# Optimization experiments

Hardware: AMD Instinct MI355X
Metric: run time of the kernel (lower is better)

Reference implementation:

```python
import jax, jax.numpy as jnp
import numpy as np

B, N, D_IN, HID = 8, 2048, 256, 64  # batch, nodes, input hidden, graph hidden (heads=1)
NEG_INF = -9e15  # matches -9000000000000000.0 in the torch code


def setup_inputs() -> dict:
    key = jax.random.key(0)
    k1, k2, k3, k4 = jax.random.split(key, 4)
    node_features = jax.random.normal(k1, (B, N, D_IN), dtype=jnp.float32)
    adj = jax.random.randint(k2, (B, N, N), 0, 2, dtype=jnp.int32)
    W = jax.random.normal(k3, (D_IN, HID), dtype=jnp.float32) / np.sqrt(D_IN).astype(np.float32)
    a = jax.random.normal(k4, (2 * HID, 1), dtype=jnp.float32) * 0.1
    return {"node_features": node_features, "adj": adj, "W": W, "a": a}


def reference(node_features, adj, W, a):
    # Wh = W(node_features): (B, N, HID)
    Wh = jnp.einsum('bnd,dh->bnh', node_features, W)
    a1 = a[:HID, 0]   # attention vector for the 'source' half of the concat
    a2 = a[HID:, 0]   # attention vector for the 'neighbor' half
    f1 = Wh @ a1      # (B, N) = Wh_i . a1
    f2 = Wh @ a2      # (B, N) = Wh_j . a2
    # e_ij = leakyrelu([Wh_i || Wh_j] . a) -- avoids the O(N^2 * 2*HID) concat
    e = jax.nn.leaky_relu(f1[:, :, None] + f2[:, None, :], negative_slope=0.2)  # (B, N, N)
    att = jnp.where(adj > 0, e, jnp.float32(NEG_INF))
    att = jax.nn.softmax(att, axis=2)
    # dropout is identity in eval / with graph_dropout=0.0
    h_prime = jnp.einsum('bij,bjh->bih', att, Wh)  # (B, N, HID)
    return h_prime
```

## Files before the change

### kernel.cpp

```cpp
#include <hip/hip_runtime.h>

#define NB 8
#define NN 2048
#define DIN 256
#define HID 64
#define JSPLIT 8

typedef __bf16 bf16x8_t __attribute__((ext_vector_type(8)));
typedef float f32x16_t __attribute__((ext_vector_type(16)));

__global__ __launch_bounds__(256) void k_wh(
    const float* __restrict__ x, const float* __restrict__ W,
    const float* __restrict__ a,
    __bf16* __restrict__ wht_hi, __bf16* __restrict__ wht_lo,
    float* __restrict__ f1, float* __restrict__ f2)
{
    __shared__ float smem[DIN * 64];
    const int t = threadIdx.x;
    const int g0 = blockIdx.x * 64;
    const int b = g0 >> 11;
    const int n0 = g0 & (NN - 1);

    const float4* x4 = (const float4*)x;
#pragma unroll
    for (int it = 0; it < 16; ++it) {
        int c = t + it * 256;
        int row = c & 63;
        int dg = c >> 6;
        float4 v = x4[(size_t)(g0 + row) * 64 + dg];
        smem[(dg * 4 + 0) * 64 + row] = v.x;
        smem[(dg * 4 + 1) * 64 + row] = v.y;
        smem[(dg * 4 + 2) * 64 + row] = v.z;
        smem[(dg * 4 + 3) * 64 + row] = v.w;
    }
    __syncthreads();

    const int hq = t & 15;
    const int rg = t >> 4;
    const float4* W4 = (const float4*)W;
    float acc[4][4] = {};
#pragma unroll 8
    for (int d = 0; d < DIN; ++d) {
        float4 wv = W4[d * 16 + hq];
        float4 xv = *(const float4*)&smem[d * 64 + rg * 4];
        float xr[4] = {xv.x, xv.y, xv.z, xv.w};
        float wk[4] = {wv.x, wv.y, wv.z, wv.w};
#pragma unroll
        for (int r = 0; r < 4; ++r)
#pragma unroll
            for (int k = 0; k < 4; ++k) acc[r][k] += xr[r] * wk[k];
    }

    float4 a1v = ((const float4*)a)[hq];
    float4 a2v = ((const float4*)a)[16 + hq];
#pragma unroll
    for (int r = 0; r < 4; ++r) {
        float p1 = acc[r][0] * a1v.x + acc[r][1] * a1v.y + acc[r][2] * a1v.z + acc[r][3] * a1v.w;
        float p2 = acc[r][0] * a2v.x + acc[r][1] * a2v.y + acc[r][2] * a2v.z + acc[r][3] * a2v.w;
#pragma unroll
        for (int m = 1; m < 16; m <<= 1) {
            p1 += __shfl_xor(p1, m);
            p2 += __shfl_xor(p2, m);
        }
        if (hq == 0) {
            f1[g0 + rg * 4 + r] = p1;
            f2[g0 + rg * 4 + r] = p2;
        }
    }

    __syncthreads();
#pragma unroll
    for (int r = 0; r < 4; ++r)
#pragma unroll
        for (int k = 0; k < 4; ++k) {
            int h = hq * 4 + k;
            int row = rg * 4 + r;
            smem[h * 64 + (((row >> 2) ^ (h & 15)) << 2) + (row & 3)] = acc[r][k];
        }
    __syncthreads();

    const int h = t >> 2;
    const int rc = t & 3;
    union { __bf16 bh[16]; uint4 u4[2]; } uh, ul;
#pragma unroll
    for (int q = 0; q < 4; ++q) {
        float4 v = *(const float4*)&smem[h * 64 + (((rc * 4 + q) ^ (h & 15)) << 2)];
        float vv[4] = {v.x, v.y, v.z, v.w};
#pragma unroll
        for (int e = 0; e < 4; ++e) {
            float val = vv[e];
            __bf16 hi = (__bf16)val;
            __bf16 lo = (__bf16)(val - (float)hi);
            uh.bh[q * 4 + e] = hi;
            ul.bh[q * 4 + e] = lo;
        }
    }
    size_t obase = (size_t)(b * HID + h) * NN + n0 + rc * 16;
    *(uint4*)&wht_hi[obase] = uh.u4[0];
    *(uint4*)&wht_hi[obase + 8] = uh.u4[1];
    *(uint4*)&wht_lo[obase] = ul.u4[0];
    *(uint4*)&wht_lo[obase + 8] = ul.u4[1];
}

__global__ __launch_bounds__(256) void k_f2max(
    const float* __restrict__ f2, float* __restrict__ f2mx)
{
    __shared__ float red[4];
    const int b = blockIdx.x, t = threadIdx.x;
    float m = -3.4e38f;
    for (int i = t; i < NN; i += 256) m = fmaxf(m, f2[b * NN + i]);
#pragma unroll
    for (int s = 1; s < 64; s <<= 1) m = fmaxf(m, __shfl_xor(m, s));
    if ((t & 63) == 0) red[t >> 6] = m;
    __syncthreads();
    if (t == 0) f2mx[b] = fmaxf(fmaxf(red[0], red[1]), fmaxf(red[2], red[3]));
}

__global__ __launch_bounds__(256, 4) void k_attn(
    const int* __restrict__ adj, const __bf16* __restrict__ wht_hi,
    const __bf16* __restrict__ wht_lo, const float* __restrict__ f1,
    const float* __restrict__ f2, const float* __restrict__ f2mx,
    float* __restrict__ accp, float* __restrict__ zp)
{
    __shared__ __bf16 whi[64 * 128];
    __shared__ __bf16 wlo[64 * 128];
    const int t = threadIdx.x;
    const int w = t >> 6, lane = t & 63;
    const int bx = blockIdx.x;
    const int js = bx & 7;
    const int it = (bx >> 3) & 15;
    const int b = bx >> 7;
    const int I0 = it * 128 + w * 32;
    const int half = lane >> 5;
    const int m32 = lane & 31;
    const int row = I0 + m32;
    const int jb0 = js * 256;

    const float f1v = f1[b * NN + row];
    float Mi = f1v + f2mx[b];
    Mi = Mi > 0.f ? Mi : 0.2f * Mi;
    const float LOG2E = 1.4426950408889634f;
    const float negMiL = -Mi * LOG2E;
    const float* f2p = f2 + b * NN;

    uint64_t mq[4];
#pragma unroll
    for (int k = 0; k < 4; ++k) mq[k] = 0;
    const int* adjbase = adj + ((size_t)b * NN + I0) * NN + jb0;
#pragma unroll 8
    for (int r = 0; r < 32; ++r) {
        const int* ar = adjbase + (size_t)r * NN;
        bool keep = (m32 == r);
#pragma unroll
        for (int k = 0; k < 4; ++k) {
            unsigned long long bal = __ballot(ar[k * 64 + lane] != 0);
            if (keep) mq[k] = bal;
        }
    }

    f32x16_t acc0, acc1;
#pragma unroll
    for (int i = 0; i < 16; ++i) { acc0[i] = 0.f; acc1[i] = 0.f; }
    float zacc = 0.f;

    for (int stg = 0; stg < 2; ++stg) {
        const int jt = jb0 + stg * 128;
        __syncthreads();
#pragma unroll
        for (int cc = 0; cc < 4; ++cc) {
            int c = t + cc * 256;
            int h = c >> 4, g = c & 15;
            int gp = g ^ (h & 15);
            size_t src = (size_t)(b * HID + h) * NN + jt + g * 8;
            *(uint4*)&whi[h * 128 + gp * 8] = *(const uint4*)&wht_hi[src];
            *(uint4*)&wlo[h * 128 + gp * 8] = *(const uint4*)&wht_lo[src];
        }
        __syncthreads();
#pragma unroll
        for (int s8 = 0; s8 < 8; ++s8) {
            const int jl = jt + s8 * 16 + half * 8;
            const uint32_t bits8 =
                (uint32_t)(mq[s8 >> 2] >> (((s8 & 3) * 16) + half * 8)) & 0xffu;
            float4 fa = *(const float4*)&f2p[jl];
            float4 fb = *(const float4*)&f2p[jl + 4];
            float fv[8] = {fa.x, fa.y, fa.z, fa.w, fb.x, fb.y, fb.z, fb.w};
            bf16x8_t ahi, alo;
#pragma unroll
            for (int jj = 0; jj < 8; ++jj) {
                float t1 = f1v + fv[jj];
                t1 = fmaxf(t1, 0.2f * t1);
                float pv = (bits8 & (1u << jj))
                         ? __builtin_amdgcn_exp2f(fmaf(t1, LOG2E, negMiL))
                         : 0.f;
                zacc += pv;
                __bf16 hb = (__bf16)pv;
                ahi[jj] = hb;
                alo[jj] = (__bf16)(pv - (float)hb);
            }
            const int gb = 2 * s8 + half;
            const int gx = gb ^ (m32 & 15);
            bf16x8_t bh0 = *(const bf16x8_t*)&whi[m32 * 128 + (gx << 3)];
            bf16x8_t bl0 = *(const bf16x8_t*)&wlo[m32 * 128 + (gx << 3)];
            bf16x8_t bh1 = *(const bf16x8_t*)&whi[(m32 + 32) * 128 + (gx << 3)];
            bf16x8_t bl1 = *(const bf16x8_t*)&wlo[(m32 + 32) * 128 + (gx << 3)];
            acc0 = __builtin_amdgcn_mfma_f32_32x32x16_bf16(ahi, bh0, acc0, 0, 0, 0);
            acc0 = __builtin_amdgcn_mfma_f32_32x32x16_bf16(ahi, bl0, acc0, 0, 0, 0);
            acc0 = __builtin_amdgcn_mfma_f32_32x32x16_bf16(alo, bh0, acc0, 0, 0, 0);
            acc1 = __builtin_amdgcn_mfma_f32_32x32x16_bf16(ahi, bh1, acc1, 0, 0, 0);
            acc1 = __builtin_amdgcn_mfma_f32_32x32x16_bf16(ahi, bl1, acc1, 0, 0, 0);
            acc1 = __builtin_amdgcn_mfma_f32_32x32x16_bf16(alo, bh1, acc1, 0, 0, 0);
        }
#pragma unroll
        for (int k = 0; k < 2; ++k) mq[k] = mq[k + 2];
    }

    float zrow = zacc + __shfl_xor(zacc, 32);
    if (lane < 32) zp[(size_t)(js * NB + b) * NN + row] = zrow;
    float* ap = accp + (size_t)(js * NB + b) * NN * HID;
#pragma unroll
    for (int r = 0; r < 16; ++r) {
        int rr = (r & 3) + 8 * (r >> 2) + 4 * half;
        ap[(size_t)(I0 + rr) * HID + m32] = acc0[r];
        ap[(size_t)(I0 + rr) * HID + m32 + 32] = acc1[r];
    }
}

__global__ __launch_bounds__(256) void k_combine(
    const float* __restrict__ accp, const float* __restrict__ zp,
    float* __restrict__ out)
{
    int gid = blockIdx.x * 256 + threadIdx.x;
    int h4 = gid & 15;
    int rowg = gid >> 4;
    float z = 0.f;
    float sx = 0.f, sy = 0.f, sz = 0.f, sw = 0.f;
#pragma unroll
    for (int js = 0; js < JSPLIT; ++js) {
        size_t base = (size_t)js * NB * NN;
        z += zp[base + rowg];
        float4 v = ((const float4*)accp)[(base + rowg) * 16 + h4];
        sx += v.x; sy += v.y; sz += v.z; sw += v.w;
    }
    float zi = 1.f / z;
    float4 o = {sx * zi, sy * zi, sz * zi, sw * zi};
    ((float4*)out)[gid] = o;
}

extern "C" void kernel_launch(void* const* d_in, const int* in_sizes, int n_in,
                              void* d_out, int out_size, void* d_ws, size_t ws_size,
                              hipStream_t stream)
{
    const float* x = (const float*)d_in[0];
    const int* adj = (const int*)d_in[1];
    const float* W = (const float*)d_in[2];
    const float* a = (const float*)d_in[3];
    float* out = (float*)d_out;
    char* ws = (char*)d_ws;

    __bf16* wht_hi = (__bf16*)(ws);
    __bf16* wht_lo = (__bf16*)(ws + (2u << 20));
    float* f1   = (float*)(ws + (4u << 20));
    float* f2   = (float*)(ws + (4u << 20) + (64u << 10));
    float* f2mx = (float*)(ws + (4u << 20) + (128u << 10));
    float* accp = (float*)(ws + (5u << 20));
    float* zp   = (float*)(ws + (37u << 20));

    hipLaunchKernelGGL(k_wh, dim3(256), dim3(256), 0, stream, x, W, a, wht_hi, wht_lo, f1, f2);
    hipLaunchKernelGGL(k_f2max, dim3(NB), dim3(256), 0, stream, f2, f2mx);
    hipLaunchKernelGGL(k_attn, dim3(1024), dim3(256), 0, stream, adj, wht_hi, wht_lo, f1, f2, f2mx, accp, zp);
    hipLaunchKernelGGL(k_combine, dim3(1024), dim3(256), 0, stream, accp, zp, out);
}
```

Measured before the change: 256.3 us.

## Software-pipeline adjacency and Wh tile loads with double-buffered shared memory

```diff
diff --git a/kernel.cpp b/kernel.cpp
--- a/kernel.cpp
+++ b/kernel.cpp
@@ -122,8 +122,8 @@
     const float* __restrict__ f2, const float* __restrict__ f2mx,
     float* __restrict__ accp, float* __restrict__ zp)
 {
-    __shared__ __bf16 whi[64 * 128];
-    __shared__ __bf16 wlo[64 * 128];
+    __shared__ __bf16 whi[2][64 * 64];
+    __shared__ __bf16 wlo[2][64 * 64];
     const int t = threadIdx.x;
     const int w = t >> 6, lane = t & 63;
     const int bx = blockIdx.x;
@@ -143,44 +143,62 @@
     const float negMiL = -Mi * LOG2E;
     const float* f2p = f2 + b * NN;
 
-    uint64_t mq[4];
-#pragma unroll
-    for (int k = 0; k < 4; ++k) mq[k] = 0;
+    const int h0 = t >> 3, g0 = t & 7;
+    const int h1 = (t + 256) >> 3, g1 = t & 7;
+    const int dst0 = h0 * 64 + ((g0 ^ (h0 & 7)) << 3);
+    const int dst1 = h1 * 64 + ((g1 ^ (h1 & 7)) << 3);
+    const __bf16* hi_s0 = wht_hi + (size_t)(b * HID + h0) * NN + jb0 + g0 * 8;
+    const __bf16* hi_s1 = wht_hi + (size_t)(b * HID + h1) * NN + jb0 + g1 * 8;
+    const __bf16* lo_s0 = wht_lo + (size_t)(b * HID + h0) * NN + jb0 + g0 * 8;
+    const __bf16* lo_s1 = wht_lo + (size_t)(b * HID + h1) * NN + jb0 + g1 * 8;
+
     const int* adjbase = adj + ((size_t)b * NN + I0) * NN + jb0;
-#pragma unroll 8
-    for (int r = 0; r < 32; ++r) {
-        const int* ar = adjbase + (size_t)r * NN;
-        bool keep = (m32 == r);
-#pragma unroll
-        for (int k = 0; k < 4; ++k) {
-            unsigned long long bal = __ballot(ar[k * 64 + lane] != 0);
-            if (keep) mq[k] = bal;
-        }
-    }
 
     f32x16_t acc0, acc1;
 #pragma unroll
     for (int i = 0; i < 16; ++i) { acc0[i] = 0.f; acc1[i] = 0.f; }
     float zacc = 0.f;
 
-    for (int stg = 0; stg < 2; ++stg) {
-        const int jt = jb0 + stg * 128;
-        __syncthreads();
-#pragma unroll
-        for (int cc = 0; cc < 4; ++cc) {
-            int c = t + cc * 256;
-            int h = c >> 4, g = c & 15;
-            int gp = g ^ (h & 15);
-            size_t src = (size_t)(b * HID + h) * NN + jt + g * 8;
-            *(uint4*)&whi[h * 128 + gp * 8] = *(const uint4*)&wht_hi[src];
-            *(uint4*)&wlo[h * 128 + gp * 8] = *(const uint4*)&wht_lo[src];
-        }
-        __syncthreads();
-#pragma unroll
-        for (int s8 = 0; s8 < 8; ++s8) {
+    int A[32];
+#pragma unroll
+    for (int r = 0; r < 32; ++r) A[r] = adjbase[(size_t)r * NN + lane];
+    {
+        uint4 th0 = *(const uint4*)&hi_s0[0];
+        uint4 th1 = *(const uint4*)&hi_s1[0];
+        uint4 tl0 = *(const uint4*)&lo_s0[0];
+        uint4 tl1 = *(const uint4*)&lo_s1[0];
+        *(uint4*)&whi[0][dst0] = th0;
+        *(uint4*)&whi[0][dst1] = th1;
+        *(uint4*)&wlo[0][dst0] = tl0;
+        *(uint4*)&wlo[0][dst1] = tl1;
+    }
+    __syncthreads();
+
+#pragma unroll
+    for (int c = 0; c < 4; ++c) {
+        const int p = c & 1, np = p ^ 1;
+        uint64_t my = 0;
+#pragma unroll
+        for (int r = 0; r < 32; ++r) {
+            unsigned long long bal = __ballot(A[r] != 0);
+            if (m32 == r) my = bal;
+        }
+        uint4 th0, th1, tl0, tl1;
+        if (c < 3) {
+            const int jn = (c + 1) * 64;
+#pragma unroll
+            for (int r = 0; r < 32; ++r)
+                A[r] = adjbase[(size_t)r * NN + jn + lane];
+            th0 = *(const uint4*)&hi_s0[jn];
+            th1 = *(const uint4*)&hi_s1[jn];
+            tl0 = *(const uint4*)&lo_s0[jn];
+            tl1 = *(const uint4*)&lo_s1[jn];
+        }
+        const int jt = jb0 + c * 64;
+#pragma unroll
+        for (int s8 = 0; s8 < 4; ++s8) {
             const int jl = jt + s8 * 16 + half * 8;
-            const uint32_t bits8 =
-                (uint32_t)(mq[s8 >> 2] >> (((s8 & 3) * 16) + half * 8)) & 0xffu;
+            const uint32_t bits8 = (uint32_t)(my >> (s8 * 16 + half * 8)) & 0xffu;
             float4 fa = *(const float4*)&f2p[jl];
             float4 fb = *(const float4*)&f2p[jl + 4];
             float fv[8] = {fa.x, fa.y, fa.z, fa.w, fb.x, fb.y, fb.z, fb.w};
@@ -197,12 +215,11 @@
                 ahi[jj] = hb;
                 alo[jj] = (__bf16)(pv - (float)hb);
             }
-            const int gb = 2 * s8 + half;
-            const int gx = gb ^ (m32 & 15);
-            bf16x8_t bh0 = *(const bf16x8_t*)&whi[m32 * 128 + (gx << 3)];
-            bf16x8_t bl0 = *(const bf16x8_t*)&wlo[m32 * 128 + (gx << 3)];
-            bf16x8_t bh1 = *(const bf16x8_t*)&whi[(m32 + 32) * 128 + (gx << 3)];
-            bf16x8_t bl1 = *(const bf16x8_t*)&wlo[(m32 + 32) * 128 + (gx << 3)];
+            const int gx = (2 * s8 + half) ^ (m32 & 7);
+            bf16x8_t bh0 = *(const bf16x8_t*)&whi[p][m32 * 64 + (gx << 3)];
+            bf16x8_t bl0 = *(const bf16x8_t*)&wlo[p][m32 * 64 + (gx << 3)];
+            bf16x8_t bh1 = *(const bf16x8_t*)&whi[p][(m32 + 32) * 64 + (gx << 3)];
+            bf16x8_t bl1 = *(const bf16x8_t*)&wlo[p][(m32 + 32) * 64 + (gx << 3)];
             acc0 = __builtin_amdgcn_mfma_f32_32x32x16_bf16(ahi, bh0, acc0, 0, 0, 0);
             acc0 = __builtin_amdgcn_mfma_f32_32x32x16_bf16(ahi, bl0, acc0, 0, 0, 0);
             acc0 = __builtin_amdgcn_mfma_f32_32x32x16_bf16(alo, bh0, acc0, 0, 0, 0);
@@ -210,8 +227,13 @@
             acc1 = __builtin_amdgcn_mfma_f32_32x32x16_bf16(ahi, bl1, acc1, 0, 0, 0);
             acc1 = __builtin_amdgcn_mfma_f32_32x32x16_bf16(alo, bh1, acc1, 0, 0, 0);
         }
-#pragma unroll
-        for (int k = 0; k < 2; ++k) mq[k] = mq[k + 2];
+        if (c < 3) {
+            *(uint4*)&whi[np][dst0] = th0;
+            *(uint4*)&whi[np][dst1] = th1;
+            *(uint4*)&wlo[np][dst0] = tl0;
+            *(uint4*)&wlo[np][dst1] = tl1;
+            __syncthreads();
+        }
     }
 
     float zrow = zacc + __shfl_xor(zacc, 32);
```

New measurement: 341.8 us. 1.33x slower.

## Use single fp16 MFMA instead of split-bf16 and prepack adjacency bitmask

Applied to the files above, without the earlier changes.

```diff
diff --git a/kernel.cpp b/kernel.cpp
--- a/kernel.cpp
+++ b/kernel.cpp
@@ -6,13 +6,13 @@
 #define HID 64
 #define JSPLIT 8
 
-typedef __bf16 bf16x8_t __attribute__((ext_vector_type(8)));
+typedef _Float16 f16x8_t __attribute__((ext_vector_type(8)));
 typedef float f32x16_t __attribute__((ext_vector_type(16)));
 
 __global__ __launch_bounds__(256) void k_wh(
     const float* __restrict__ x, const float* __restrict__ W,
     const float* __restrict__ a,
-    __bf16* __restrict__ wht_hi, __bf16* __restrict__ wht_lo,
+    _Float16* __restrict__ wht,
     float* __restrict__ f1, float* __restrict__ f2)
 {
     __shared__ float smem[DIN * 64];
@@ -81,25 +81,18 @@
 
     const int h = t >> 2;
     const int rc = t & 3;
-    union { __bf16 bh[16]; uint4 u4[2]; } uh, ul;
+    union { _Float16 fh[16]; uint4 u4[2]; } uh;
 #pragma unroll
     for (int q = 0; q < 4; ++q) {
         float4 v = *(const float4*)&smem[h * 64 + (((rc * 4 + q) ^ (h & 15)) << 2)];
-        float vv[4] = {v.x, v.y, v.z, v.w};
-#pragma unroll
-        for (int e = 0; e < 4; ++e) {
-            float val = vv[e];
-            __bf16 hi = (__bf16)val;
-            __bf16 lo = (__bf16)(val - (float)hi);
-            uh.bh[q * 4 + e] = hi;
-            ul.bh[q * 4 + e] = lo;
-        }
+        uh.fh[q * 4 + 0] = (_Float16)v.x;
+        uh.fh[q * 4 + 1] = (_Float16)v.y;
+        uh.fh[q * 4 + 2] = (_Float16)v.z;
+        uh.fh[q * 4 + 3] = (_Float16)v.w;
     }
     size_t obase = (size_t)(b * HID + h) * NN + n0 + rc * 16;
-    *(uint4*)&wht_hi[obase] = uh.u4[0];
-    *(uint4*)&wht_hi[obase + 8] = uh.u4[1];
-    *(uint4*)&wht_lo[obase] = ul.u4[0];
-    *(uint4*)&wht_lo[obase + 8] = ul.u4[1];
+    *(uint4*)&wht[obase] = uh.u4[0];
+    *(uint4*)&wht[obase + 8] = uh.u4[1];
 }
 
 __global__ __launch_bounds__(256) void k_f2max(
@@ -116,14 +109,33 @@
     if (t == 0) f2mx[b] = fmaxf(fmaxf(red[0], red[1]), fmaxf(red[2], red[3]));
 }
 
+__global__ __launch_bounds__(256) void k_pack(
+    const int* __restrict__ adj, unsigned long long* __restrict__ mb)
+{
+    const int t = threadIdx.x;
+    const int lane = t & 63;
+    const int wave = blockIdx.x * 4 + (t >> 6);
+#pragma unroll
+    for (int rr = 0; rr < 2; ++rr) {
+        const int row = wave * 2 + rr;
+        const int* ar = adj + (size_t)row * NN;
+        unsigned long long myw = 0;
+#pragma unroll
+        for (int k = 0; k < 32; ++k) {
+            unsigned long long bal = __ballot(ar[k * 64 + lane] != 0);
+            if ((lane & 31) == k) myw = bal;
+        }
+        if (lane < 32) mb[(size_t)row * 32 + lane] = myw;
+    }
+}
+
 __global__ __launch_bounds__(256, 4) void k_attn(
-    const int* __restrict__ adj, const __bf16* __restrict__ wht_hi,
-    const __bf16* __restrict__ wht_lo, const float* __restrict__ f1,
-    const float* __restrict__ f2, const float* __restrict__ f2mx,
+    const unsigned long long* __restrict__ mb, const _Float16* __restrict__ wht,
+    const float* __restrict__ f1, const float* __restrict__ f2,
+    const float* __restrict__ f2mx,
     float* __restrict__ accp, float* __restrict__ zp)
 {
-    __shared__ __bf16 whi[64 * 128];
-    __shared__ __bf16 wlo[64 * 128];
+    __shared__ _Float16 whx[64 * 128];
     const int t = threadIdx.x;
     const int w = t >> 6, lane = t & 63;
     const int bx = blockIdx.x;
@@ -143,19 +155,12 @@
     const float negMiL = -Mi * LOG2E;
     const float* f2p = f2 + b * NN;
 
-    uint64_t mq[4];
-#pragma unroll
-    for (int k = 0; k < 4; ++k) mq[k] = 0;
-    const int* adjbase = adj + ((size_t)b * NN + I0) * NN + jb0;
-#pragma unroll 8
-    for (int r = 0; r < 32; ++r) {
-        const int* ar = adjbase + (size_t)r * NN;
-        bool keep = (m32 == r);
-#pragma unroll
-        for (int k = 0; k < 4; ++k) {
-            unsigned long long bal = __ballot(ar[k * 64 + lane] != 0);
-            if (keep) mq[k] = bal;
-        }
+    const unsigned long long* mrow = mb + (size_t)(b * NN + row) * 32 + js * 4;
+    unsigned long long m[4];
+    {
+        ulonglong2 q0 = *(const ulonglong2*)mrow;
+        ulonglong2 q1 = *(const ulonglong2*)(mrow + 2);
+        m[0] = q0.x; m[1] = q0.y; m[2] = q1.x; m[3] = q1.y;
     }
 
     f32x16_t acc0, acc1;
@@ -163,28 +168,28 @@
     for (int i = 0; i < 16; ++i) { acc0[i] = 0.f; acc1[i] = 0.f; }
     float zacc = 0.f;
 
+#pragma unroll
     for (int stg = 0; stg < 2; ++stg) {
         const int jt = jb0 + stg * 128;
-        __syncthreads();
+        if (stg) __syncthreads();
 #pragma unroll
         for (int cc = 0; cc < 4; ++cc) {
             int c = t + cc * 256;
             int h = c >> 4, g = c & 15;
             int gp = g ^ (h & 15);
             size_t src = (size_t)(b * HID + h) * NN + jt + g * 8;
-            *(uint4*)&whi[h * 128 + gp * 8] = *(const uint4*)&wht_hi[src];
-            *(uint4*)&wlo[h * 128 + gp * 8] = *(const uint4*)&wht_lo[src];
+            *(uint4*)&whx[h * 128 + gp * 8] = *(const uint4*)&wht[src];
         }
         __syncthreads();
 #pragma unroll
         for (int s8 = 0; s8 < 8; ++s8) {
             const int jl = jt + s8 * 16 + half * 8;
             const uint32_t bits8 =
-                (uint32_t)(mq[s8 >> 2] >> (((s8 & 3) * 16) + half * 8)) & 0xffu;
+                (uint32_t)(m[stg * 2 + (s8 >> 2)] >> (((s8 & 3) * 16) + half * 8)) & 0xffu;
             float4 fa = *(const float4*)&f2p[jl];
             float4 fb = *(const float4*)&f2p[jl + 4];
             float fv[8] = {fa.x, fa.y, fa.z, fa.w, fb.x, fb.y, fb.z, fb.w};
-            bf16x8_t ahi, alo;
+            f16x8_t ah;
 #pragma unroll
             for (int jj = 0; jj < 8; ++jj) {
                 float t1 = f1v + fv[jj];
@@ -192,26 +197,16 @@
                 float pv = (bits8 & (1u << jj))
                          ? __builtin_amdgcn_exp2f(fmaf(t1, LOG2E, negMiL))
                          : 0.f;
-                zacc += pv;
-                __bf16 hb = (__bf16)pv;
-                ahi[jj] = hb;
-                alo[jj] = (__bf16)(pv - (float)hb);
+                _Float16 ph = (_Float16)pv;
+                ah[jj] = ph;
+                zacc += (float)ph;
             }
-            const int gb = 2 * s8 + half;
-            const int gx = gb ^ (m32 & 15);
-            bf16x8_t bh0 = *(const bf16x8_t*)&whi[m32 * 128 + (gx << 3)];
-            bf16x8_t bl0 = *(const bf16x8_t*)&wlo[m32 * 128 + (gx << 3)];
-            bf16x8_t bh1 = *(const bf16x8_t*)&whi[(m32 + 32) * 128 + (gx << 3)];
-            bf16x8_t bl1 = *(const bf16x8_t*)&wlo[(m32 + 32) * 128 + (gx << 3)];
-            acc0 = __builtin_amdgcn_mfma_f32_32x32x16_bf16(ahi, bh0, acc0, 0, 0, 0);
-            acc0 = __builtin_amdgcn_mfma_f32_32x32x16_bf16(ahi, bl0, acc0, 0, 0, 0);
-            acc0 = __builtin_amdgcn_mfma_f32_32x32x16_bf16(alo, bh0, acc0, 0, 0, 0);
-            acc1 = __builtin_amdgcn_mfma_f32_32x32x16_bf16(ahi, bh1, acc1, 0, 0, 0);
-            acc1 = __builtin_amdgcn_mfma_f32_32x32x16_bf16(ahi, bl1, acc1, 0, 0, 0);
-            acc1 = __builtin_amdgcn_mfma_f32_32x32x16_bf16(alo, bh1, acc1, 0, 0, 0);
-        }
-#pragma unroll
-        for (int k = 0; k < 2; ++k) mq[k] = mq[k + 2];
+            const int gx = (2 * s8 + half) ^ (m32 & 15);
+            f16x8_t b0 = *(const f16x8_t*)&whx[m32 * 128 + (gx << 3)];
+            f16x8_t b1 = *(const f16x8_t*)&whx[(m32 + 32) * 128 + (gx << 3)];
+            acc0 = __builtin_amdgcn_mfma_f32_32x32x16_f16(ah, b0, acc0, 0, 0, 0);
+            acc1 = __builtin_amdgcn_mfma_f32_32x32x16_f16(ah, b1, acc1, 0, 0, 0);
+        }
     }
 
     float zrow = zacc + __shfl_xor(zacc, 32);
@@ -257,16 +252,17 @@
     float* out = (float*)d_out;
     char* ws = (char*)d_ws;
 
-    __bf16* wht_hi = (__bf16*)(ws);
-    __bf16* wht_lo = (__bf16*)(ws + (2u << 20));
-    float* f1   = (float*)(ws + (4u << 20));
-    float* f2   = (float*)(ws + (4u << 20) + (64u << 10));
-    float* f2mx = (float*)(ws + (4u << 20) + (128u << 10));
-    float* accp = (float*)(ws + (5u << 20));
-    float* zp   = (float*)(ws + (37u << 20));
-
-    hipLaunchKernelGGL(k_wh, dim3(256), dim3(256), 0, stream, x, W, a, wht_hi, wht_lo, f1, f2);
+    _Float16* wht = (_Float16*)(ws);
+    float* f1   = (float*)(ws + (2u << 20));
+    float* f2   = (float*)(ws + (2u << 20) + (64u << 10));
+    float* f2mx = (float*)(ws + (2u << 20) + (128u << 10));
+    unsigned long long* mbuf = (unsigned long long*)(ws + (3u << 20));
+    float* accp = (float*)(ws + (8u << 20));
+    float* zp   = (float*)(ws + (40u << 20));
+
+    hipLaunchKernelGGL(k_pack, dim3(2048), dim3(256), 0, stream, adj, mbuf);
+    hipLaunchKernelGGL(k_wh, dim3(256), dim3(256), 0, stream, x, W, a, wht, f1, f2);
     hipLaunchKernelGGL(k_f2max, dim3(NB), dim3(256), 0, stream, f2, f2mx);
-    hipLaunchKernelGGL(k_attn, dim3(1024), dim3(256), 0, stream, adj, wht_hi, wht_lo, f1, f2, f2mx, accp, zp);
+    hipLaunchKernelGGL(k_attn, dim3(1024), dim3(256), 0, stream, mbuf, wht, f1, f2, f2mx, accp, zp);
     hipLaunchKernelGGL(k_combine, dim3(1024), dim3(256), 0, stream, accp, zp, out);
 }
```

Result: no change. 260.3 us (+1.6%).
